# Optimization experiments

Measured on AMD Instinct MI355X. Metric: run time of the kernel, lower is better.

## Reference

```python
import jax, jax.numpy as jnp
import numpy as np

TEMPERATURE = 0.5
EPS = 1e-8  # torch CosineSimilarity eps


def setup_inputs() -> dict:
    key = jax.random.key(0)
    k1, k2, k3 = jax.random.split(key, 3)
    N, D, C = 8192, 128, 1000
    embed = jax.random.normal(k1, (N, D), dtype=jnp.float32)
    proxy = jax.random.normal(k2, (N, D), dtype=jnp.float32)
    label = jax.random.randint(k3, (N,), 0, C, dtype=jnp.int64)
    return {"embed": embed, "proxy": proxy, "label": label}


def _l2_normalize(x):
    # mirrors torch CosineSimilarity: x / max(||x||, eps)
    n = jnp.sqrt(jnp.sum(x * x, axis=-1, keepdims=True))
    return x / jnp.maximum(n, EPS)


def reference(embed, proxy, label):
    N = embed.shape[0]
    en = _l2_normalize(embed)                       # [N, D]
    # pairwise cosine sim via normalize+matmul (instead of O(N^2 D) broadcast)
    sim = jnp.exp(jnp.einsum("nd,md->nm", en, en) / TEMPERATURE)  # [N, N]
    offdiag = 1.0 - jnp.eye(N, dtype=sim.dtype)
    sim = sim * offdiag                             # zero diag == remove-diag for row sums
    # positives: same label, excluding self
    same = (label[:, None] == label[None, :]).astype(sim.dtype) * offdiag
    pos_sum = jnp.sum(sim * same, axis=1)           # [N]
    # embed-to-proxy similarity
    pn = _l2_normalize(proxy)
    emb2proxy = jnp.exp(jnp.sum(en * pn, axis=-1) / TEMPERATURE)  # [N]
    numerator = emb2proxy + pos_sum
    denominator = emb2proxy + jnp.sum(sim, axis=1)
    return -jnp.mean(jnp.log(numerator / denominator))
```

## Files before the change

### kernel.cpp

```cpp
#include <hip/hip_runtime.h>
#include <hip/hip_bf16.h>

#define N_ROWS 8192
#define DIM    128
#define NCHUNK 16
#define CHUNKC (N_ROWS / NCHUNK)
#define NT     (CHUNKC / 32)

#define ENSCALE 1.6986436f

typedef __attribute__((ext_vector_type(8)))  short short8;
typedef __attribute__((ext_vector_type(16))) float f32x16;
typedef __attribute__((address_space(3))) void lds_void;
typedef const __attribute__((address_space(1))) void g_void;

__device__ inline unsigned short f2bf(float f) {
    unsigned u = __float_as_uint(f);
    unsigned r = (u + 0x7FFFu + ((u >> 16) & 1u)) >> 16;
    return (unsigned short)r;
}
__device__ inline float bf2f(unsigned short u) {
    return __uint_as_float(((unsigned)u) << 16);
}

__global__ __launch_bounds__(256) void norm_kernel(
    const float* __restrict__ embed, const float* __restrict__ proxy,
    short* __restrict__ enb, float* __restrict__ e2p)
{
    int wave = threadIdx.x >> 6, lane = threadIdx.x & 63;
    int row = blockIdx.x * 4 + wave;

    const float2 ev = *(const float2*)(embed + row * DIM + lane * 2);
    float ss = ev.x * ev.x + ev.y * ev.y;
#pragma unroll
    for (int m = 1; m < 64; m <<= 1) ss += __shfl_xor(ss, m, 64);
    float inv_e = 1.0f / fmaxf(sqrtf(ss), 1e-8f);
    float ex = ev.x * inv_e, ey = ev.y * inv_e;

    const float2 pv = *(const float2*)(proxy + row * DIM + lane * 2);
    float ps = pv.x * pv.x + pv.y * pv.y;
#pragma unroll
    for (int m = 1; m < 64; m <<= 1) ps += __shfl_xor(ps, m, 64);
    float inv_p = 1.0f / fmaxf(sqrtf(ps), 1e-8f);

    float dot = ex * (pv.x * inv_p) + ey * (pv.y * inv_p);
#pragma unroll
    for (int m = 1; m < 64; m <<= 1) dot += __shfl_xor(dot, m, 64);

    ushort2 st; st.x = f2bf(ex * ENSCALE); st.y = f2bf(ey * ENSCALE);
    *(ushort2*)(enb + row * DIM + lane * 2) = st;
    if (lane == 0) e2p[row] = __expf(2.0f * dot);
}

__global__ __launch_bounds__(256, 4) void simsum_kernel(
    const short* __restrict__ enb, float* __restrict__ ptot)
{
    __shared__ __align__(16) char lds[2 * 8192];
    const int tid = threadIdx.x;
    const int wave = tid >> 6, lane = tid & 63;
    const int cl = lane & 31;
    const int hi = lane >> 5;
    const int wrbase = blockIdx.x * 128 + wave * 32;
    const int cbase0 = blockIdx.y * CHUNKC;

    const int sc = tid >> 4;
    const int sj = (tid & 15) ^ sc;

    auto stage = [&](int buf, int cb) {
        const short* s0 = enb + (size_t)(cb + sc) * DIM + sj * 8;
        const short* s1 = enb + (size_t)(cb + 16 + sc) * DIM + sj * 8;
        char* d0 = lds + buf * 8192 + wave * 1024;
        char* d1 = d0 + 4096;
        __builtin_amdgcn_global_load_lds((g_void*)s0, (lds_void*)d0, 16, 0, 0);
        __builtin_amdgcn_global_load_lds((g_void*)s1, (lds_void*)d1, 16, 0, 0);
    };

    short8 rres[8];
    const short* arow = enb + (size_t)(wrbase + cl) * DIM + hi * 8;
#pragma unroll
    for (int kk = 0; kk < 8; kk++)
        rres[kk] = *(const short8*)(arow + kk * 16);

    float tot[16];
#pragma unroll
    for (int r = 0; r < 16; r++) tot[r] = 0.f;

    int cur = 0;
    stage(0, cbase0);
    __syncthreads();

#pragma unroll 1
    for (int t = 0; t < NT; t++) {
        if (t + 1 < NT) stage(cur ^ 1, cbase0 + (t + 1) * 32);

        const char* base = lds + cur * 8192 + cl * 256;
        short8 b[8];
#pragma unroll
        for (int kk = 0; kk < 8; kk++) {
            int off = ((kk * 2 + hi) ^ (cl & 15)) * 16;
            b[kk] = *(const short8*)(base + off);
        }

        f32x16 c = {};
#pragma unroll
        for (int kk = 0; kk < 8; kk++)
            c = __builtin_amdgcn_mfma_f32_32x32x16_bf16(b[kk], rres[kk], c, 0, 0, 0);

        const int cb = cbase0 + t * 32;
        if (cb == wrbase) {
#pragma unroll
            for (int r = 0; r < 16; r++) {
                int colr = (r & 3) + 4 * hi + 8 * (r >> 2);
                float s = __builtin_amdgcn_exp2f(c[r]);
                tot[r] += (colr == cl) ? 0.f : s;
            }
        } else {
#pragma unroll
            for (int r = 0; r < 16; r++)
                tot[r] += __builtin_amdgcn_exp2f(c[r]);
        }

        __syncthreads();
        cur ^= 1;
    }

    float s = 0.f;
#pragma unroll
    for (int r = 0; r < 16; r++) s += tot[r];
    s += __shfl_xor(s, 32, 64);
    if (hi == 0)
        ptot[blockIdx.y * N_ROWS + wrbase + cl] = s;
}

__global__ __launch_bounds__(256) void pos_kernel(
    const short* __restrict__ enb, const int* __restrict__ label,
    float* __restrict__ posr)
{
    int wave = threadIdx.x >> 6, lane = threadIdx.x & 63;
    int row = blockIdx.x * 4 + wave;
    int mylab = label[row];

    ushort2 e2 = *(const ushort2*)(enb + (size_t)row * DIM + lane * 2);
    float ei0 = bf2f(e2.x), ei1 = bf2f(e2.y);

    float acc = 0.f;
    for (int ch = 0; ch < N_ROWS / 64; ch++) {
        int j = ch * 64 + lane;
        bool m = (label[j] == mylab) && (j != row);
        unsigned long long mask = __ballot(m);
        while (mask) {
            int jj = ch * 64 + (__ffsll(mask) - 1);
            mask &= mask - 1;
            ushort2 f2 = *(const ushort2*)(enb + (size_t)jj * DIM + lane * 2);
            float d = ei0 * bf2f(f2.x) + ei1 * bf2f(f2.y);
#pragma unroll
            for (int s = 1; s < 64; s <<= 1) d += __shfl_xor(d, s, 64);
            acc += __builtin_amdgcn_exp2f(d);
        }
    }
    if (lane == 0) posr[row] = acc;
}

__global__ __launch_bounds__(256) void loss_partial_kernel(
    const float* __restrict__ e2p, const float* __restrict__ ptot,
    const float* __restrict__ posr, float* __restrict__ pl)
{
    int i = blockIdx.x * 256 + threadIdx.x;
    float tot = 0.f;
#pragma unroll
    for (int c = 0; c < NCHUNK; c++) tot += ptot[c * N_ROWS + i];
    float e = e2p[i];
    float v = __logf((e + posr[i]) / (e + tot));
#pragma unroll
    for (int m = 1; m < 64; m <<= 1) v += __shfl_xor(v, m, 64);
    __shared__ float red[4];
    int wave = threadIdx.x >> 6, lane = threadIdx.x & 63;
    if (lane == 0) red[wave] = v;
    __syncthreads();
    if (threadIdx.x == 0) pl[blockIdx.x] = red[0] + red[1] + red[2] + red[3];
}

__global__ void loss_final_kernel(const float* __restrict__ pl,
                                  float* __restrict__ out)
{
    float v = (threadIdx.x < 32) ? pl[threadIdx.x] : 0.f;
#pragma unroll
    for (int m = 1; m < 64; m <<= 1) v += __shfl_xor(v, m, 64);
    if (threadIdx.x == 0) out[0] = -v / (float)N_ROWS;
}

extern "C" void kernel_launch(void* const* d_in, const int* in_sizes, int n_in,
                              void* d_out, int out_size, void* d_ws, size_t ws_size,
                              hipStream_t stream) {
    const float* embed = (const float*)d_in[0];
    const float* proxy = (const float*)d_in[1];
    const int*   label = (const int*)d_in[2];
    float* out = (float*)d_out;

    char* ws = (char*)d_ws;
    short* enb  = (short*)ws;
    float* e2p  = (float*)(ws + 2u * N_ROWS * DIM);
    float* ptot = e2p + N_ROWS;
    float* posr = ptot + NCHUNK * N_ROWS;
    float* pl   = posr + N_ROWS;

    hipLaunchKernelGGL(norm_kernel, dim3(N_ROWS / 4), dim3(256), 0, stream,
                       embed, proxy, enb, e2p);
    hipLaunchKernelGGL(simsum_kernel, dim3(N_ROWS / 128, NCHUNK), dim3(256), 0, stream,
                       enb, ptot);
    hipLaunchKernelGGL(pos_kernel, dim3(N_ROWS / 4), dim3(256), 0, stream,
                       enb, label, posr);
    hipLaunchKernelGGL(loss_partial_kernel, dim3(N_ROWS / 256), dim3(256), 0, stream,
                       e2p, ptot, posr, pl);
    hipLaunchKernelGGL(loss_final_kernel, dim3(1), dim3(64), 0, stream, pl, out);
}
```

Measured before the change: 59.14 us.

## Enlarge simsum register tile to 64 rows per wave and stage 64-column phases

Each wave now holds two 32-row A fragments in registers and reuses every LDS-loaded B fragment for two MFMA chains, halving LDS reads per flop. Each pipeline phase stages 64 columns instead of 32, so there are half as many barriers. The grid halves to 32x16 blocks and launch bounds drop to 2 blocks per CU, trading occupancy for register reuse. The exp2 accumulators are folded into 4-wide partial sums to save registers.

```diff
diff --git a/kernel.cpp b/kernel.cpp
--- a/kernel.cpp
+++ b/kernel.cpp
@@ -6,6 +6,7 @@
 #define NCHUNK 16
 #define CHUNKC (N_ROWS / NCHUNK)
 #define NT     (CHUNKC / 32)
+#define NPH    (NT / 2)
 
 #define ENSCALE 1.6986436f
 
@@ -52,84 +53,100 @@
     if (lane == 0) e2p[row] = __expf(2.0f * dot);
 }
 
-__global__ __launch_bounds__(256, 4) void simsum_kernel(
+#define DOTILE(buf, tt, cb_tile)                                               \
+    {                                                                          \
+        const char* base_ = lds + (buf) * 16384 + (tt) * 8192 + cl * 256;      \
+        short8 b[8];                                                           \
+        _Pragma("unroll")                                                      \
+        for (int kk = 0; kk < 8; kk++) {                                       \
+            int off = ((kk * 2 + hi) ^ (cl & 15)) * 16;                        \
+            b[kk] = *(const short8*)(base_ + off);                             \
+        }                                                                      \
+        f32x16 c0 = {}, c1 = {};                                               \
+        _Pragma("unroll")                                                      \
+        for (int kk = 0; kk < 8; kk++) {                                       \
+            c0 = __builtin_amdgcn_mfma_f32_32x32x16_bf16(b[kk], rres0[kk], c0, \
+                                                         0, 0, 0);             \
+            c1 = __builtin_amdgcn_mfma_f32_32x32x16_bf16(b[kk], rres1[kk], c1, \
+                                                         0, 0, 0);             \
+        }                                                                      \
+        const bool d0_ = ((cb_tile) == wrbase);                                \
+        const bool d1_ = ((cb_tile) == wrbase + 32);                           \
+        _Pragma("unroll")                                                      \
+        for (int r = 0; r < 16; r++) {                                         \
+            int colr = (r & 3) + 4 * hi + 8 * (r >> 2);                        \
+            float s0 = __builtin_amdgcn_exp2f(c0[r]);                          \
+            float s1 = __builtin_amdgcn_exp2f(c1[r]);                          \
+            s0 = (d0_ && colr == cl) ? 0.f : s0;                               \
+            s1 = (d1_ && colr == cl) ? 0.f : s1;                               \
+            tot0[r & 3] += s0;                                                 \
+            tot1[r & 3] += s1;                                                 \
+        }                                                                      \
+    }
+
+__global__ __launch_bounds__(256, 2) void simsum_kernel(
     const short* __restrict__ enb, float* __restrict__ ptot)
 {
-    __shared__ __align__(16) char lds[2 * 8192];
+    __shared__ __align__(16) char lds[2 * 16384];
     const int tid = threadIdx.x;
-    const int wave = tid >> 6, lane = tid & 63;
+    const int wave = tid >> 6;
+    const int lane = tid & 63;
     const int cl = lane & 31;
     const int hi = lane >> 5;
-    const int wrbase = blockIdx.x * 128 + wave * 32;
+    const int wrbase = blockIdx.x * 256 + wave * 64;
     const int cbase0 = blockIdx.y * CHUNKC;
 
     const int sc = tid >> 4;
     const int sj = (tid & 15) ^ sc;
 
-    auto stage = [&](int buf, int cb) {
-        const short* s0 = enb + (size_t)(cb + sc) * DIM + sj * 8;
-        const short* s1 = enb + (size_t)(cb + 16 + sc) * DIM + sj * 8;
-        char* d0 = lds + buf * 8192 + wave * 1024;
-        char* d1 = d0 + 4096;
-        __builtin_amdgcn_global_load_lds((g_void*)s0, (lds_void*)d0, 16, 0, 0);
-        __builtin_amdgcn_global_load_lds((g_void*)s1, (lds_void*)d1, 16, 0, 0);
+    auto stage = [&](int buf, int ph) {
+        const int cb = cbase0 + ph * 64;
+        char* dbase = lds + buf * 16384 + wave * 1024;
+#pragma unroll
+        for (int h = 0; h < 4; h++) {
+            const short* src = enb + (size_t)(cb + h * 16 + sc) * DIM + sj * 8;
+            __builtin_amdgcn_global_load_lds((g_void*)src,
+                                             (lds_void*)(dbase + h * 4096),
+                                             16, 0, 0);
+        }
     };
 
-    short8 rres[8];
-    const short* arow = enb + (size_t)(wrbase + cl) * DIM + hi * 8;
-#pragma unroll
-    for (int kk = 0; kk < 8; kk++)
-        rres[kk] = *(const short8*)(arow + kk * 16);
-
-    float tot[16];
-#pragma unroll
-    for (int r = 0; r < 16; r++) tot[r] = 0.f;
+    short8 rres0[8], rres1[8];
+    {
+        const short* a0 = enb + (size_t)(wrbase + cl) * DIM + hi * 8;
+        const short* a1 = enb + (size_t)(wrbase + 32 + cl) * DIM + hi * 8;
+#pragma unroll
+        for (int kk = 0; kk < 8; kk++) {
+            rres0[kk] = *(const short8*)(a0 + kk * 16);
+            rres1[kk] = *(const short8*)(a1 + kk * 16);
+        }
+    }
+
+    float tot0[4] = {0.f, 0.f, 0.f, 0.f};
+    float tot1[4] = {0.f, 0.f, 0.f, 0.f};
 
     int cur = 0;
-    stage(0, cbase0);
+    stage(0, 0);
     __syncthreads();
 
 #pragma unroll 1
-    for (int t = 0; t < NT; t++) {
-        if (t + 1 < NT) stage(cur ^ 1, cbase0 + (t + 1) * 32);
-
-        const char* base = lds + cur * 8192 + cl * 256;
-        short8 b[8];
-#pragma unroll
-        for (int kk = 0; kk < 8; kk++) {
-            int off = ((kk * 2 + hi) ^ (cl & 15)) * 16;
-            b[kk] = *(const short8*)(base + off);
-        }
-
-        f32x16 c = {};
-#pragma unroll
-        for (int kk = 0; kk < 8; kk++)
-            c = __builtin_amdgcn_mfma_f32_32x32x16_bf16(b[kk], rres[kk], c, 0, 0, 0);
-
-        const int cb = cbase0 + t * 32;
-        if (cb == wrbase) {
-#pragma unroll
-            for (int r = 0; r < 16; r++) {
-                int colr = (r & 3) + 4 * hi + 8 * (r >> 2);
-                float s = __builtin_amdgcn_exp2f(c[r]);
-                tot[r] += (colr == cl) ? 0.f : s;
-            }
-        } else {
-#pragma unroll
-            for (int r = 0; r < 16; r++)
-                tot[r] += __builtin_amdgcn_exp2f(c[r]);
-        }
-
+    for (int ph = 0; ph < NPH; ph++) {
+        if (ph + 1 < NPH) stage(cur ^ 1, ph + 1);
+        const int cb = cbase0 + ph * 64;
+        DOTILE(cur, 0, cb);
+        DOTILE(cur, 1, cb + 32);
         __syncthreads();
         cur ^= 1;
     }
 
-    float s = 0.f;
-#pragma unroll
-    for (int r = 0; r < 16; r++) s += tot[r];
-    s += __shfl_xor(s, 32, 64);
-    if (hi == 0)
-        ptot[blockIdx.y * N_ROWS + wrbase + cl] = s;
+    float t0 = tot0[0] + tot0[1] + tot0[2] + tot0[3];
+    float t1 = tot1[0] + tot1[1] + tot1[2] + tot1[3];
+    t0 += __shfl_xor(t0, 32, 64);
+    t1 += __shfl_xor(t1, 32, 64);
+    if (hi == 0) {
+        ptot[blockIdx.y * N_ROWS + wrbase + cl] = t0;
+        ptot[blockIdx.y * N_ROWS + wrbase + 32 + cl] = t1;
+    }
 }
 
 __global__ __launch_bounds__(256) void pos_kernel(
@@ -206,7 +223,7 @@
 
     hipLaunchKernelGGL(norm_kernel, dim3(N_ROWS / 4), dim3(256), 0, stream,
                        embed, proxy, enb, e2p);
-    hipLaunchKernelGGL(simsum_kernel, dim3(N_ROWS / 128, NCHUNK), dim3(256), 0, stream,
+    hipLaunchKernelGGL(simsum_kernel, dim3(N_ROWS / 256, NCHUNK), dim3(256), 0, stream,
                        enb, ptot);
     hipLaunchKernelGGL(pos_kernel, dim3(N_ROWS / 4), dim3(256), 0, stream,
                        enb, label, posr);
```

Measured after the change: 57.73 us. 2.4% less time.
